# Kernel tuning notes

Measured on AMD Instinct MI355X. Metric: run time of the kernel, lower is better.

Reference implementation:

```python
import jax, jax.numpy as jnp
import numpy as np

B, S, D, H = 2, 2048, 2048, 16
DH = D // H
EPS = 1e-5


def layernorm(x, gamma, beta):
    mu = jnp.mean(x, axis=-1, keepdims=True)
    var = jnp.var(x, axis=-1, keepdims=True)
    return (x - mu) * jax.lax.rsqrt(var + EPS) * gamma + beta


def setup_inputs() -> dict:
    key = jax.random.key(0)
    ks = jax.random.split(key, 10)
    sc = 1.0 / np.sqrt(D)
    return {
        "x": jax.random.normal(ks[0], (B, S, D), dtype=jnp.float32),
        "wq": jax.random.normal(ks[1], (D, D), dtype=jnp.float32) * sc,
        "bq": jnp.zeros((D,), jnp.float32),
        "wk": jax.random.normal(ks[2], (D, D), dtype=jnp.float32) * sc,
        "bk": jnp.zeros((D,), jnp.float32),
        "wv": jax.random.normal(ks[3], (D, D), dtype=jnp.float32) * sc,
        "bv": jnp.zeros((D,), jnp.float32),
        "wf": jax.random.normal(ks[4], (D, D), dtype=jnp.float32) * sc,
        "bf": jnp.zeros((D,), jnp.float32),
        "gamma": jnp.ones((D,), jnp.float32),
        "beta": jnp.zeros((D,), jnp.float32),
    }


def reference(x, wq, bq, wk, bk, wv, bv, wf, bf, gamma, beta):
    q = x @ wq + bq
    k = x @ wk + bk
    v = x @ wv + bv
    # split: [B,S,D] -> [B,H,S,DH]
    split = lambda t: t.reshape(B, S, H, DH).transpose(0, 2, 1, 3)
    q, k, v = split(q), split(k), split(v)
    s = jnp.einsum("bhqd,bhkd->bhqk", q, k) / np.sqrt(DH)
    p = jax.nn.softmax(s, axis=-1)
    o = jnp.einsum("bhqk,bhkd->bhqd", p, v)
    # faithful to original buggy concat: flat view of [B,H,S,DH] as [B,S,H*DH]
    o = o.reshape(B, S, H * DH)
    vb = o
    h1 = layernorm(o + x, gamma, beta)
    h2 = h1 @ wf + bf
    out = layernorm(h2 + vb, gamma, beta)
    return out
```

## Files before the change

### kernel.cpp

```cpp
#include <hip/hip_runtime.h>


#define B_ 2
#define S_ 2048
#define D_ 2048
#define H_ 16
#define DH_ 128

typedef __attribute__((ext_vector_type(8))) short s16x8;
typedef __attribute__((ext_vector_type(8))) unsigned short u16x8;
typedef __attribute__((ext_vector_type(4))) float f32x4;
typedef __attribute__((ext_vector_type(4))) unsigned short u16x4;

#define MFMA16(a, b, c) __builtin_amdgcn_mfma_f32_16x16x32_bf16(a, b, c, 0, 0, 0)

__device__ inline unsigned short f2bf(float f) {
  union { float f; unsigned u; } x; x.f = f;
  unsigned r = (x.u + 0x7fffu + ((x.u >> 16) & 1u)) >> 16;
  return (unsigned short)r;
}
__device__ inline float bf2f(unsigned short u) {
  union { unsigned u; float f; } x; x.u = ((unsigned)u) << 16;
  return x.f;
}
__device__ inline unsigned pack2bf(float a, float b) {
  unsigned ua = __builtin_bit_cast(unsigned, a) + 0x8000u;
  unsigned ub = __builtin_bit_cast(unsigned, b) + 0x8000u;
  return __builtin_amdgcn_perm(ub, ua, 0x07060302u);
}

__device__ inline void gld_lds16(const void* g, void* l) {
  __builtin_amdgcn_global_load_lds(
      (__attribute__((address_space(1))) void*)g,
      (__attribute__((address_space(3))) void*)l, 16, 0, 0);
}

__global__ __launch_bounds__(256) void prep_kernel(
    const float* __restrict__ x, unsigned short* __restrict__ xb,
    const float* __restrict__ w0, const float* __restrict__ w1,
    const float* __restrict__ w2, const float* __restrict__ w3,
    unsigned short* __restrict__ o0, unsigned short* __restrict__ o1,
    unsigned short* __restrict__ o2, unsigned short* __restrict__ o3) {
  int z = blockIdx.z;
  int t = threadIdx.x;
  if (z == 4) {
    int base = (blockIdx.y * 32 + blockIdx.x) * 16384 + t * 4;
#pragma unroll
    for (int p = 0; p < 16; ++p) {
      int i = base + p * 1024;
      float4 v = *(const float4*)&x[i];
      u16x4 o;
      o.x = f2bf(v.x); o.y = f2bf(v.y); o.z = f2bf(v.z); o.w = f2bf(v.w);
      *(u16x4*)&xb[i] = o;
    }
    return;
  }
  const float* W = z == 0 ? w0 : z == 1 ? w1 : z == 2 ? w2 : w3;
  unsigned short* WT = z == 0 ? o0 : z == 1 ? o1 : z == 2 ? o2 : o3;
  int n0 = blockIdx.x * 64, k0 = blockIdx.y * 128;
  int cl = t & 15, rw = t >> 4;
  int kb = k0 + rw * 8, nb = n0 + cl * 4;
  float4 f[8];
#pragma unroll
  for (int r = 0; r < 8; ++r) f[r] = *(const float4*)&W[(kb + r) * D_ + nb];
#define TPOSE(comp, i)                                                      \
  {                                                                         \
    u16x8 o = {f2bf(f[0].comp), f2bf(f[1].comp), f2bf(f[2].comp),           \
               f2bf(f[3].comp), f2bf(f[4].comp), f2bf(f[5].comp),           \
               f2bf(f[6].comp), f2bf(f[7].comp)};                           \
    *(u16x8*)&WT[(nb + i) * D_ + kb] = o;                                   \
  }
  TPOSE(x, 0) TPOSE(y, 1) TPOSE(z, 2) TPOSE(w, 3)
#undef TPOSE
}

__global__ __launch_bounds__(256) void gemm_qkv_kernel(
    const unsigned short* __restrict__ A, const unsigned short* __restrict__ W0,
    const unsigned short* __restrict__ W1, const unsigned short* __restrict__ W2,
    const float* __restrict__ b0, const float* __restrict__ b1,
    const float* __restrict__ b2, unsigned short* __restrict__ Qb,
    unsigned short* __restrict__ Kb, unsigned short* __restrict__ Vt,
    float qscale) {
  __shared__ short As[128 * 64];
  __shared__ short Bs[128 * 64];
  int wi = blockIdx.x >> 4;
  int n0 = (blockIdx.x & 15) * 128;
  const unsigned short* BT = wi == 0 ? W0 : wi == 1 ? W1 : W2;
  const float* bias = wi == 0 ? b0 : wi == 1 ? b1 : b2;
  float oscale = wi == 0 ? qscale : 1.0f;

  int t = threadIdx.x, lane = t & 63, w = t >> 6;
  int nl = lane & 15, q = lane >> 4;
  int m0 = blockIdx.y * 128;
  int wr = (w >> 1) * 64, wc = (w & 1) * 64;
  int swz = nl & 7;

  f32x4 acc[4][4];
  f32x4 z4 = {0.f, 0.f, 0.f, 0.f};
#pragma unroll
  for (int i = 0; i < 4; ++i)
#pragma unroll
    for (int j = 0; j < 4; ++j) acc[i][j] = z4;

  for (int kk = 0; kk < 2048; kk += 64) {
    __syncthreads();
#pragma unroll
    for (int i2 = 0; i2 < 4; ++i2) {
      int c = t + 256 * i2;
      int row = c >> 3, dc = (c & 7) ^ (row & 7);
      gld_lds16(&A[(m0 + row) * 2048 + kk + dc * 8], &As[c * 8]);
      gld_lds16(&BT[(n0 + row) * 2048 + kk + dc * 8], &Bs[c * 8]);
    }
    __syncthreads();
#pragma unroll
    for (int kc = 0; kc < 2; ++kc) {
      s16x8 af[4], bf[4];
#pragma unroll
      for (int i = 0; i < 4; ++i)
        af[i] = *(const s16x8*)&As[(wr + i * 16 + nl) * 64 +
                                   (((kc << 2) + q) ^ swz) * 8];
#pragma unroll
      for (int j = 0; j < 4; ++j)
        bf[j] = *(const s16x8*)&Bs[(wc + j * 16 + nl) * 64 +
                                   (((kc << 2) + q) ^ swz) * 8];
#pragma unroll
      for (int i = 0; i < 4; ++i)
#pragma unroll
        for (int j = 0; j < 4; ++j) acc[i][j] = MFMA16(af[i], bf[j], acc[i][j]);
    }
  }
#pragma unroll
  for (int i = 0; i < 4; ++i)
#pragma unroll
    for (int j = 0; j < 4; ++j) {
      int row = m0 + wr + i * 16 + q * 4;
      int col = n0 + wc + j * 16 + nl;
      float bv = bias[col];
      float v[4];
#pragma unroll
      for (int r = 0; r < 4; ++r) v[r] = (acc[i][j][r] + bv) * oscale;
      if (wi == 2) {
        unsigned d0 = pack2bf(v[0], v[1]), d1 = pack2bf(v[2], v[3]);
        long idx = ((long)(((row >> 11) * 16 + (col >> 7)) * 128 + (col & 127))) * 2048 +
                   (row & 2047);
        *(uint2*)&Vt[idx] = (uint2){d0, d1};
      } else {
        unsigned short* out = wi == 0 ? Qb : Kb;
#pragma unroll
        for (int r = 0; r < 4; ++r)
          out[(row + r) * 2048 + col] = f2bf(v[r]);
      }
    }
}

__global__ __launch_bounds__(256, 4) void gemm_ff_kernel(
    const unsigned short* __restrict__ A, const unsigned short* __restrict__ BT,
    const float* __restrict__ bias, unsigned short* __restrict__ Cout) {
  __shared__ short As[128 * 64];
  __shared__ short Bs[64 * 64];
  int t = threadIdx.x, lane = t & 63, w = t >> 6;
  int nl = lane & 15, q = lane >> 4;
  int m0 = blockIdx.y * 128, n0 = blockIdx.x * 64;
  int wr = (w >> 1) * 64, wc = (w & 1) * 32;
  int swz = nl & 7;

  f32x4 acc[4][2];
  f32x4 z4 = {0.f, 0.f, 0.f, 0.f};
#pragma unroll
  for (int i = 0; i < 4; ++i) {
    acc[i][0] = z4;
    acc[i][1] = z4;
  }

  for (int kk = 0; kk < 2048; kk += 64) {
    __syncthreads();
#pragma unroll
    for (int i2 = 0; i2 < 4; ++i2) {
      int c = t + 256 * i2;
      int row = c >> 3, dc = (c & 7) ^ (row & 7);
      gld_lds16(&A[(m0 + row) * 2048 + kk + dc * 8], &As[c * 8]);
    }
#pragma unroll
    for (int i2 = 0; i2 < 2; ++i2) {
      int c = t + 256 * i2;
      int row = c >> 3, dc = (c & 7) ^ (row & 7);
      gld_lds16(&BT[(n0 + row) * 2048 + kk + dc * 8], &Bs[c * 8]);
    }
    __syncthreads();
#pragma unroll
    for (int kc = 0; kc < 2; ++kc) {
      s16x8 af[4], bf0, bf1;
#pragma unroll
      for (int i = 0; i < 4; ++i)
        af[i] = *(const s16x8*)&As[(wr + i * 16 + nl) * 64 +
                                   (((kc << 2) + q) ^ swz) * 8];
      bf0 = *(const s16x8*)&Bs[(wc + nl) * 64 + (((kc << 2) + q) ^ swz) * 8];
      bf1 = *(const s16x8*)&Bs[(wc + 16 + nl) * 64 + (((kc << 2) + q) ^ swz) * 8];
#pragma unroll
      for (int i = 0; i < 4; ++i) {
        acc[i][0] = MFMA16(af[i], bf0, acc[i][0]);
        acc[i][1] = MFMA16(af[i], bf1, acc[i][1]);
      }
    }
  }
#pragma unroll
  for (int i = 0; i < 4; ++i)
#pragma unroll
    for (int j = 0; j < 2; ++j) {
      int row = m0 + wr + i * 16 + q * 4;
      int col = n0 + wc + j * 16 + nl;
      float bv = bias[col];
#pragma unroll
      for (int r = 0; r < 4; ++r)
        Cout[(row + r) * 2048 + col] = f2bf(acc[i][j][r] + bv);
    }
}

__global__ __launch_bounds__(256, 2) void attn_kernel(
    const unsigned short* __restrict__ Q, const unsigned short* __restrict__ K,
    const unsigned short* __restrict__ VT, unsigned short* __restrict__ O) {
  __shared__ short KsA[8192], KsB[8192];
  __shared__ short VsA[8192], VsB[8192];
  __shared__ short Ps[8192];
  int t = threadIdx.x, lane = t & 63, w = t >> 6;
  int nl = lane & 15, q = lane >> 4;
  int i = blockIdx.x;
  int qb = i >> 5;
  int bh = (i & 7) + 8 * ((i >> 3) & 3);
  int b = bh >> 4, h = bh & 15;

  s16x8 qf[2][4];
  int qrow = b * S_ + qb * 128 + w * 32;
#pragma unroll
  for (int t2 = 0; t2 < 2; ++t2)
#pragma unroll
    for (int kc = 0; kc < 4; ++kc)
      qf[t2][kc] = *(const s16x8*)&Q[(qrow + t2 * 16 + nl) * D_ + h * DH_ + kc * 32 + q * 8];

  f32x4 z4 = {0.f, 0.f, 0.f, 0.f};
  f32x4 accO[2][8];
  f32x4 l4[2] = {z4, z4};
#pragma unroll
  for (int t2 = 0; t2 < 2; ++t2)
#pragma unroll
    for (int n8 = 0; n8 < 8; ++n8) accO[t2][n8] = z4;

  int swz = nl & 7;

  const unsigned short* kp[4];
  const unsigned short* vp[4];
#pragma unroll
  for (int i2 = 0; i2 < 4; ++i2) {
    int c = t + 256 * i2;
    int kc = c >> 8, rem = c & 255, s = rem >> 2, dc = rem & 3;
    kp[i2] = K + (long)(b * S_ + s) * D_ + h * DH_ + kc * 32 + dc * 8;
    int d = c >> 3, cp = c & 7, cs = cp ^ (d & 7);
    vp[i2] = VT + (long)(bh * DH_ + d) * S_ + cs * 8;
  }

#define STAGE(bufK, bufV)                           \
  {                                                 \
    _Pragma("unroll") for (int i2 = 0; i2 < 4; ++i2) { \
      gld_lds16(kp[i2], &bufK[(t + 256 * i2) * 8]); \
      gld_lds16(vp[i2], &bufV[(t + 256 * i2) * 8]); \
      kp[i2] += 64 * D_;                            \
      vp[i2] += 64;                                 \
    }                                               \
  }

  auto compute = [&](const short* Ks, const short* Vs) {
    f32x4 accS[2][4];
#pragma unroll
    for (int t2 = 0; t2 < 2; ++t2)
#pragma unroll
      for (int n = 0; n < 4; ++n) accS[t2][n] = z4;
#pragma unroll
    for (int kc = 0; kc < 4; ++kc) {
      s16x8 kf[4];
#pragma unroll
      for (int n = 0; n < 4; ++n)
        kf[n] = *(const s16x8*)&Ks[kc * 2048 + (n * 16 + nl) * 32 + q * 8];
#pragma unroll
      for (int t2 = 0; t2 < 2; ++t2)
#pragma unroll
        for (int n = 0; n < 4; ++n)
          accS[t2][n] = MFMA16(kf[n], qf[t2][kc], accS[t2][n]);
    }

#pragma unroll
    for (int t2 = 0; t2 < 2; ++t2) {
      int prow = (w * 32 + t2 * 16 + nl) * 64;
#pragma unroll
      for (int n = 0; n < 4; ++n) {
#pragma unroll
        for (int r = 0; r < 4; ++r)
          accS[t2][n][r] = __builtin_amdgcn_exp2f(accS[t2][n][r] - 16.0f);
        l4[t2] += accS[t2][n];
        unsigned d0 = pack2bf(accS[t2][n][0], accS[t2][n][1]);
        unsigned d1 = pack2bf(accS[t2][n][2], accS[t2][n][3]);
        int c8 = q + 4 * n;
        int off = prow + (((c8 >> 1) ^ swz) * 8 + (c8 & 1) * 4);
        *(uint2*)&Ps[off] = (uint2){d0, d1};
      }
    }

#pragma unroll
    for (int ks = 0; ks < 2; ++ks) {
      s16x8 pf[2];
#pragma unroll
      for (int t2 = 0; t2 < 2; ++t2)
        pf[t2] = *(const s16x8*)&Ps[(w * 32 + t2 * 16 + nl) * 64 + ((4 * ks + q) ^ swz) * 8];
#pragma unroll
      for (int n8 = 0; n8 < 8; ++n8) {
        int d = n8 * 16 + nl;
        int cs = ks * 4 + q;
        int ci = d * 8 + (cs ^ (d & 7));
        s16x8 vf = *(const s16x8*)&Vs[ci * 8];
#pragma unroll
        for (int t2 = 0; t2 < 2; ++t2)
          accO[t2][n8] = MFMA16(vf, pf[t2], accO[t2][n8]);
      }
    }
  };

  STAGE(KsA, VsA);
  for (int it = 0; it < 32; it += 2) {
    __syncthreads();
    STAGE(KsB, VsB);
    compute(KsA, VsA);
    __syncthreads();
    if (it + 2 < 32) STAGE(KsA, VsA);
    compute(KsB, VsB);
  }
#undef STAGE

#pragma unroll
  for (int t2 = 0; t2 < 2; ++t2) {
    float l = (l4[t2][0] + l4[t2][1]) + (l4[t2][2] + l4[t2][3]);
    l += __shfl_xor(l, 16);
    l += __shfl_xor(l, 32);
    float inv = 1.0f / l;
    int s = qb * 128 + w * 32 + t2 * 16 + nl;
    unsigned short* orow = &O[((long)(bh * S_ + s)) * DH_];
#pragma unroll
    for (int n8 = 0; n8 < 8; ++n8) {
      unsigned d0 = pack2bf(accO[t2][n8][0] * inv, accO[t2][n8][1] * inv);
      unsigned d1 = pack2bf(accO[t2][n8][2] * inv, accO[t2][n8][3] * inv);
      *(uint2*)&orow[n8 * 16 + q * 4] = (uint2){d0, d1};
    }
  }
}

template <int OUTBF, int INBF>
__global__ __launch_bounds__(256) void ln_kernel(
    const void* __restrict__ Ain, const unsigned short* __restrict__ Ob,
    const float* __restrict__ gamma, const float* __restrict__ beta,
    void* __restrict__ out) {
  int row = blockIdx.x, t = threadIdx.x;
  int lane = t & 63, w = t >> 6;
  float v[8], s = 0.f, s2 = 0.f;
#pragma unroll
  for (int p = 0; p < 8; ++p) {
    int c = t + p * 256;
    float a = INBF ? bf2f(((const unsigned short*)Ain)[row * D_ + c])
                   : ((const float*)Ain)[row * D_ + c];
    a += bf2f(Ob[row * D_ + c]);
    v[p] = a; s += a; s2 += a * a;
  }
#pragma unroll
  for (int mk = 32; mk >= 1; mk >>= 1) {
    s += __shfl_xor(s, mk);
    s2 += __shfl_xor(s2, mk);
  }
  __shared__ float red[8];
  if (lane == 0) { red[w * 2] = s; red[w * 2 + 1] = s2; }
  __syncthreads();
  s = red[0] + red[2] + red[4] + red[6];
  s2 = red[1] + red[3] + red[5] + red[7];
  float mu = s * (1.0f / D_);
  float var = s2 * (1.0f / D_) - mu * mu;
  float rs = rsqrtf(var + 1e-5f);
#pragma unroll
  for (int p = 0; p < 8; ++p) {
    int c = t + p * 256;
    float o = (v[p] - mu) * rs * gamma[c] + beta[c];
    if (OUTBF)
      ((unsigned short*)out)[row * D_ + c] = f2bf(o);
    else
      ((float*)out)[row * D_ + c] = o;
  }
}

extern "C" void kernel_launch(void* const* d_in, const int* in_sizes, int n_in,
                              void* d_out, int out_size, void* d_ws, size_t ws_size,
                              hipStream_t stream) {
  const float* x     = (const float*)d_in[0];
  const float* wq    = (const float*)d_in[1];
  const float* bq    = (const float*)d_in[2];
  const float* wk    = (const float*)d_in[3];
  const float* bk    = (const float*)d_in[4];
  const float* wv    = (const float*)d_in[5];
  const float* bv    = (const float*)d_in[6];
  const float* wf    = (const float*)d_in[7];
  const float* bfb   = (const float*)d_in[8];
  const float* gamma = (const float*)d_in[9];
  const float* beta  = (const float*)d_in[10];

  unsigned short* ws  = (unsigned short*)d_ws;
  unsigned short* WqT = ws;
  unsigned short* WkT = ws + 4194304;
  unsigned short* WvT = ws + 8388608;
  unsigned short* WfT = ws + 12582912;
  unsigned short* Xb  = ws + 16777216;
  unsigned short* Qb  = ws + 25165824;
  unsigned short* Kb  = ws + 33554432;
  unsigned short* Vt  = ws + 41943040;
  unsigned short* Ob  = Xb;
  unsigned short* H1  = Kb;
  unsigned short* H2b = Vt;

  const float scl2 = 0.08838834764831845f * 1.4426950408889634f;

  dim3 blk(256);
  prep_kernel<<<dim3(32, 16, 5), blk, 0, stream>>>(
      x, Xb, wq, wk, wv, wf, WqT, WkT, WvT, WfT);

  gemm_qkv_kernel<<<dim3(48, 32), blk, 0, stream>>>(
      Xb, WqT, WkT, WvT, bq, bk, bv, Qb, Kb, Vt, scl2);

  attn_kernel<<<dim3(512), blk, 0, stream>>>(Qb, Kb, Vt, Ob);

  ln_kernel<1, 0><<<dim3(4096), blk, 0, stream>>>(x, Ob, gamma, beta, (void*)H1);
  gemm_ff_kernel<<<dim3(32, 32), blk, 0, stream>>>(H1, WfT, bfb, H2b);
  ln_kernel<0, 1><<<dim3(4096), blk, 0, stream>>>(H2b, Ob, gamma, beta, d_out);
}
```

Before: 417.7 us.

## Swizzle K tile LDS layout in attention and vectorize layernorm loads/stores

The attention kernel's K staging changes from a kc-major chunked layout to a row-major 128-wide LDS layout with an XOR swizzle on 16-byte chunks. Fragment reads use the matching swizzle, which is meant to cut LDS bank conflicts and make the global-to-LDS copies more contiguous. Separately, the layernorm kernel now has each thread handle 8 contiguous elements with vector loads and stores, replacing strided scalar accesses. The changed column mapping per thread must stay consistent with the reductions, which it does because the sums are order-independent.

```diff
diff --git a/kernel.cpp b/kernel.cpp
--- a/kernel.cpp
+++ b/kernel.cpp
@@ -252,10 +252,14 @@
 #pragma unroll
   for (int i2 = 0; i2 < 4; ++i2) {
     int c = t + 256 * i2;
-    int kc = c >> 8, rem = c & 255, s = rem >> 2, dc = rem & 3;
-    kp[i2] = K + (long)(b * S_ + s) * D_ + h * DH_ + kc * 32 + dc * 8;
-    int d = c >> 3, cp = c & 7, cs = cp ^ (d & 7);
-    vp[i2] = VT + (long)(bh * DH_ + d) * S_ + cs * 8;
+    {
+      int r = c >> 4, cp = c & 15, j = cp ^ (r & 7);
+      kp[i2] = K + (long)(b * S_ + r) * D_ + h * DH_ + j * 8;
+    }
+    {
+      int d = c >> 3, cp = c & 7, cs = cp ^ (d & 7);
+      vp[i2] = VT + (long)(bh * DH_ + d) * S_ + cs * 8;
+    }
   }
 
 #define STAGE(bufK, bufV)                           \
@@ -279,7 +283,8 @@
       s16x8 kf[4];
 #pragma unroll
       for (int n = 0; n < 4; ++n)
-        kf[n] = *(const s16x8*)&Ks[kc * 2048 + (n * 16 + nl) * 32 + q * 8];
+        kf[n] = *(const s16x8*)&Ks[(n * 16 + nl) * 128 +
+                                   (((kc << 2) + q) ^ swz) * 8];
 #pragma unroll
       for (int t2 = 0; t2 < 2; ++t2)
 #pragma unroll
@@ -358,15 +363,25 @@
     void* __restrict__ out) {
   int row = blockIdx.x, t = threadIdx.x;
   int lane = t & 63, w = t >> 6;
+  int c0 = t * 8;
   float v[8], s = 0.f, s2 = 0.f;
-#pragma unroll
-  for (int p = 0; p < 8; ++p) {
-    int c = t + p * 256;
-    float a = INBF ? bf2f(((const unsigned short*)Ain)[row * D_ + c])
-                   : ((const float*)Ain)[row * D_ + c];
-    a += bf2f(Ob[row * D_ + c]);
-    v[p] = a; s += a; s2 += a * a;
-  }
+  {
+    u16x8 ov = *(const u16x8*)&Ob[row * D_ + c0];
+    if (INBF) {
+      u16x8 av = *(const u16x8*)&((const unsigned short*)Ain)[row * D_ + c0];
+#pragma unroll
+      for (int p = 0; p < 8; ++p) v[p] = bf2f(av[p]) + bf2f(ov[p]);
+    } else {
+      float4 a0 = *(const float4*)&((const float*)Ain)[row * D_ + c0];
+      float4 a1 = *(const float4*)&((const float*)Ain)[row * D_ + c0 + 4];
+      v[0] = a0.x + bf2f(ov[0]); v[1] = a0.y + bf2f(ov[1]);
+      v[2] = a0.z + bf2f(ov[2]); v[3] = a0.w + bf2f(ov[3]);
+      v[4] = a1.x + bf2f(ov[4]); v[5] = a1.y + bf2f(ov[5]);
+      v[6] = a1.z + bf2f(ov[6]); v[7] = a1.w + bf2f(ov[7]);
+    }
+  }
+#pragma unroll
+  for (int p = 0; p < 8; ++p) { s += v[p]; s2 += v[p] * v[p]; }
 #pragma unroll
   for (int mk = 32; mk >= 1; mk >>= 1) {
     s += __shfl_xor(s, mk);
@@ -380,14 +395,25 @@
   float mu = s * (1.0f / D_);
   float var = s2 * (1.0f / D_) - mu * mu;
   float rs = rsqrtf(var + 1e-5f);
-#pragma unroll
-  for (int p = 0; p < 8; ++p) {
-    int c = t + p * 256;
-    float o = (v[p] - mu) * rs * gamma[c] + beta[c];
-    if (OUTBF)
-      ((unsigned short*)out)[row * D_ + c] = f2bf(o);
-    else
-      ((float*)out)[row * D_ + c] = o;
+  float4 g0 = *(const float4*)&gamma[c0];
+  float4 g1 = *(const float4*)&gamma[c0 + 4];
+  float4 be0 = *(const float4*)&beta[c0];
+  float4 be1 = *(const float4*)&beta[c0 + 4];
+  float o[8];
+  o[0] = (v[0] - mu) * rs * g0.x + be0.x; o[1] = (v[1] - mu) * rs * g0.y + be0.y;
+  o[2] = (v[2] - mu) * rs * g0.z + be0.z; o[3] = (v[3] - mu) * rs * g0.w + be0.w;
+  o[4] = (v[4] - mu) * rs * g1.x + be1.x; o[5] = (v[5] - mu) * rs * g1.y + be1.y;
+  o[6] = (v[6] - mu) * rs * g1.z + be1.z; o[7] = (v[7] - mu) * rs * g1.w + be1.w;
+  if (OUTBF) {
+    u16x8 ob;
+#pragma unroll
+    for (int p = 0; p < 8; ++p) ob[p] = f2bf(o[p]);
+    *(u16x8*)&((unsigned short*)out)[row * D_ + c0] = ob;
+  } else {
+    float4 o0 = {o[0], o[1], o[2], o[3]};
+    float4 o1 = {o[4], o[5], o[6], o[7]};
+    *(float4*)&((float*)out)[row * D_ + c0] = o0;
+    *(float4*)&((float*)out)[row * D_ + c0 + 4] = o1;
   }
 }
 
```

Result: no change. 422.9 us (+1.3%).
